# Optimization experiments

Measured on AMD Instinct MI355X. Metric: run time of the kernel, lower is better.

Reference implementation:

```python
import jax, jax.numpy as jnp
import numpy as np

# Constants from the torch module __init__
FACE_INDS = np.array([[0, 1, 2, 3], [0, 4, 2, 6], [0, 1, 4, 5],
                      [1, 3, 5, 7], [2, 3, 6, 7], [4, 5, 6, 7]])  # (6,4)
N_GRID = 11
N_POINTS = N_GRID * N_GRID        # 121
N_FACE = 6
N_KP_HAND = 21
N_CONTACTS = 10
ITA = 0.2
IND1 = np.array([0, 1, 2, 3])
IND2 = np.array([1, 2, 3, 0])


def _bilinear_grid():
    # grid[p, k] = bilinear weights for the 4 face corners, p over 11x11 (u,v)
    g = []
    for u in np.linspace(0.0, 1.0, N_GRID):
        for v in np.linspace(0.0, 1.0, N_GRID):
            g.append([v * (1 - u), v * u, (1 - v) * (1 - u), u * (1 - v)])
    return jnp.asarray(np.array(g, dtype=np.float32))  # (121, 4)


def setup_inputs() -> dict:
    key = jax.random.key(0)
    poses = jax.random.normal(key, (8192, N_KP_HAND + 8, 3), dtype=jnp.float32)
    return {"poses": poses}


def affinity_loss(poses):
    bs = poses.shape[0]
    hand = poses[:, :N_KP_HAND, :]          # (bs, 21, 3)
    obj = poses[:, N_KP_HAND:, :]           # (bs, 8, 3)

    # --- sample_face_points: bilinear sample 121 pts on each of the 6 faces ---
    grid = _bilinear_grid().astype(poses.dtype)        # (121, 4)
    faces = obj[:, FACE_INDS, :]                        # (bs, 6, 4, 3)
    face_points = jnp.einsum('bfkc,pk->bfpc', faces, grid)  # (bs, 6, 121, 3)
    obj_pts = face_points.reshape(bs, N_FACE * N_POINTS, 3)  # (bs, 726, 3)

    xx = jnp.sum(hand * hand, axis=-1)                  # (bs, 21)
    yy = jnp.sum(obj_pts * obj_pts, axis=-1)            # (bs, 726)
    zz = jnp.einsum('bic,bjc->bij', hand, obj_pts)      # (bs, 21, 726)
    pdist = jnp.sqrt(xx[:, :, None] + yy[:, None, :] - 2.0 * zz + 1e-6)
    pdist = pdist.reshape(bs, N_KP_HAND, N_FACE, N_POINTS)

    # --- per (hand kp, face) nearest face point, then global top-10 contacts ---
    dist_h2f = jnp.min(pdist, axis=3)                   # (bs, 21, 6)
    idxs_h2f = jnp.argmin(pdist, axis=3)                # (bs, 21, 6)
    flat = dist_h2f.reshape(bs, N_KP_HAND * N_FACE)     # (bs, 126)
    order = jnp.argsort(flat, axis=1)[:, :N_CONTACTS]   # (bs, 10)
    dist = jnp.take_along_axis(flat, order, axis=1)     # (bs, 10)
    inds_hand = order // N_FACE
    inds_face = order % N_FACE
    b = jnp.arange(bs)[:, None]
    ind_obj = idxs_h2f[b, inds_hand, inds_face]                     # (bs, 10)
    obj_contacts = obj_pts[b, inds_face * N_POINTS + ind_obj]       # (bs, 10, 3)

    # --- get_obj_info: axis endpoints and mean edge length of the bbox ---
    points1 = obj[:, :4, :].mean(axis=1)                # (bs, 3)
    points2 = obj[:, 4:, :].mean(axis=1)                # (bs, 3)
    l1 = jnp.linalg.norm(obj[:, IND1] - obj[:, IND2], axis=-1).mean(1, keepdims=True)
    l2 = jnp.linalg.norm(obj[:, IND1 + 4] - obj[:, IND2 + 4], axis=-1).mean(1, keepdims=True)
    length = (l1 + l2) * 0.5                            # (bs, 1)

    mask1 = (dist < length * ITA).astype(poses.dtype)   # (bs, 10)
    mask = mask1[:, :, None] * mask1[:, None, :]        # (bs, 10, 10)

    direct_vec = points2 - points1                      # (bs, 3)
    dv_norm = jnp.linalg.norm(direct_vec, axis=1, keepdims=True)  # (bs, 1)
    normed_dv = direct_vec / (dv_norm + 1e-5)
    vec_contacts = obj_contacts - points1[:, None, :]   # (bs, 10, 3)
    inner = jnp.sum(direct_vec[:, None, :] * vec_contacts, axis=-1)  # (bs, 10)
    t = inner / (dv_norm + 1e-5)                        # (bs, 10)
    r = points1[:, None, :] + normed_dv[:, None, :] * t[:, :, None]  # (bs, 10, 3)
    normal_vec = obj_contacts - r
    normal_vec = normal_vec / (jnp.linalg.norm(normal_vec, axis=2, keepdims=True) + 1e-5)
    cos_sim = jnp.einsum('bic,bjc->bij', normal_vec, normal_vec)  # (bs, 10, 10)

    return (cos_sim * mask).sum() / (mask.sum() + 1.0)


def reference(poses):
    return affinity_loss(poses)
```

## Files before the change

kernel.cpp:

```cpp
#include <hip/hip_runtime.h>
#include <math.h>

#define NGRID   11
#define NPAIR   126
#define NCONT   10

#define NSUB    64
#define NBUK    128
#define WS_SUB  16
#define WS_BUK  128
#define WS_WORDS (WS_BUK + 2 * NBUK)

#define NBUCKET 256

typedef float v2f __attribute__((ext_vector_type(2)));
#define FMA2(a,b,c) __builtin_elementwise_fma((a),(b),(c))
#define MAX2(a,b)   __builtin_elementwise_max((a),(b))
#define SP2(x)      ((v2f){(x),(x)})

__device__ __constant__ int4 c_face4[6] = {
    {0,1,2,3},{0,4,2,6},{0,1,4,5},{1,3,5,7},{2,3,6,7},{4,5,6,7}};
__device__ __constant__ float c_U[NGRID] = {
    0.0f,0.1f,0.2f,0.3f,0.4f,0.5f,0.6f,0.7f,0.8f,0.9f,1.0f};

__global__ void zero_ws_kernel(float* ws, int n) {
    int t = blockIdx.x * 256 + threadIdx.x;
    if (t < n) ws[t] = 0.0f;
}

__device__ __forceinline__ void coefs_from_face(
        const float4* __restrict__ Ff, float hx, float hy, float hz,
        float& C00, float& C10, float& C01, float& C11,
        float& C20, float& C02, float& C21, float& C12, float& C22) {
    const float4 F0 = Ff[0], F1 = Ff[1], F2 = Ff[2],
                 F3 = Ff[3], F4 = Ff[4], F5 = Ff[5];
    const float hx2 = 2.0f * hx, hy2 = 2.0f * hy, hz2 = 2.0f * hz;
    const float ha2 = fmaf(hx2, F0.x, fmaf(hy2, F0.y, hz2 * F0.z));
    const float hb2 = fmaf(hx2, F1.x, fmaf(hy2, F1.y, hz2 * F1.z));
    const float hc2 = fmaf(hx2, F2.x, fmaf(hy2, F2.y, hz2 * F2.z));
    const float hd2 = fmaf(hx2, F3.x, fmaf(hy2, F3.y, hz2 * F3.z));
    C00 = ha2 - F0.w;
    C10 = hb2 - F4.x;
    C01 = hc2 - F4.y;
    C11 = hd2 - F4.z;
    C20 = -F1.w;  C02 = -F2.w;  C21 = -F4.w;  C12 = -F5.x;  C22 = -F3.w;
}

__launch_bounds__(256)
__global__ void affinity_kernel(const float* __restrict__ poses,
                                float* __restrict__ ws,
                                float* __restrict__ out,
                                int bs, int mode) {
    const int t    = threadIdx.x;
    const int half = t >> 7;
    const int t0   = t & 127;
    const int batch = blockIdx.x * 2 + half;
    const bool valid = batch < bs;

    __shared__ float    sh_pose[2][88];
    __shared__ float4   sh_face[2][36];
    __shared__ float    sh_thr[2][2];
    __shared__ int      sh_ru[2][128];
    __shared__ int      sh_cpair[2][128];
    __shared__ unsigned sh_cnt[2], sh_cnt2[2];
    __shared__ unsigned sh_key[2][128];
    __shared__ float    sh_cont[2][128][3];
    __shared__ float    sh_win[2][NCONT][3];
    __shared__ float    sh_nd[2][2];
    __shared__ int      sh_last;
    __shared__ double   sh_rn[4], sh_rd[4];

    if (valid && t0 < 87) sh_pose[half][t0] = poses[(size_t)batch * 87 + t0];
    if (t0 == 127) { sh_cnt[half] = 0u; sh_cnt2[half] = 0u; }
    __syncthreads();

    const float* hand = sh_pose[half];
    const float* obj  = sh_pose[half] + 63;

    if (valid && t0 < 6) {
        const int4 F = c_face4[t0];
        float C0[3], C1[3], C2[3], C3[3];
        #pragma unroll
        for (int c = 0; c < 3; ++c) {
            C0[c] = obj[F.x * 3 + c];
            C1[c] = obj[F.y * 3 + c];
            C2[c] = obj[F.z * 3 + c];
            C3[c] = obj[F.w * 3 + c];
        }
        float av[3], bv[3], cv[3], dv[3];
        #pragma unroll
        for (int c = 0; c < 3; ++c) {
            av[c] = C2[c];
            bv[c] = C3[c] - C2[c];
            cv[c] = C0[c] - C2[c];
            dv[c] = C1[c] - C0[c] - C3[c] + C2[c];
        }
        float aa=0.f,bb=0.f,cc=0.f,dd=0.f,ab=0.f,ac=0.f,ad=0.f,bc=0.f,bd=0.f,cd=0.f;
        #pragma unroll
        for (int c = 0; c < 3; ++c) {
            aa += av[c]*av[c]; bb += bv[c]*bv[c];
            cc += cv[c]*cv[c]; dd += dv[c]*dv[c];
            ab += av[c]*bv[c]; ac += av[c]*cv[c];
            ad += av[c]*dv[c]; bc += bv[c]*cv[c];
            bd += bv[c]*dv[c]; cd += cv[c]*dv[c];
        }
        float4* Ff = &sh_face[half][t0 * 6];
        Ff[0] = make_float4(av[0], av[1], av[2], aa);
        Ff[1] = make_float4(bv[0], bv[1], bv[2], bb);
        Ff[2] = make_float4(cv[0], cv[1], cv[2], cc);
        Ff[3] = make_float4(dv[0], dv[1], dv[2], dd);
        Ff[4] = make_float4(2.f*ab, 2.f*ac, 2.f*(ad+bc), 2.f*bd);
        Ff[5] = make_float4(2.f*cd, 0.f, 0.f, 0.f);
    }
    if (valid && t0 == 6) {
        float l1 = 0.0f, l2 = 0.0f;
        #pragma unroll
        for (int e = 0; e < 4; ++e) {
            const int a = e, b2 = (e + 1) & 3;
            {
                const float dx = obj[a*3+0]-obj[b2*3+0];
                const float dy = obj[a*3+1]-obj[b2*3+1];
                const float dz = obj[a*3+2]-obj[b2*3+2];
                l1 += sqrtf(dx*dx + dy*dy + dz*dz);
            }
            {
                const float dx = obj[(a+4)*3+0]-obj[(b2+4)*3+0];
                const float dy = obj[(a+4)*3+1]-obj[(b2+4)*3+1];
                const float dz = obj[(a+4)*3+2]-obj[(b2+4)*3+2];
                l2 += sqrtf(dx*dx + dy*dy + dz*dz);
            }
        }
        l1 *= 0.25f; l2 *= 0.25f;
        const float L02 = (l1 + l2) * 0.5f * 0.2f;
        sh_thr[half][0] = L02 * L02 - 1e-6f + 1e-2f;
        sh_thr[half][1] = L02;
    }
    __syncthreads();

    if (valid && t0 < NPAIR) {
        const int i = t0 / 6;
        const int f = t0 - i * 6;
        const float hx = hand[i*3+0], hy = hand[i*3+1], hz = hand[i*3+2];
        const float xx = hx*hx + hy*hy + hz*hz;
        float C00,C10,C01,C11,C20,C02,C21,C12,C22;
        coefs_from_face(&sh_face[half][f*6], hx, hy, hz,
                        C00,C10,C01,C11,C20,C02,C21,C12,C22);

        const float U[NGRID] = {0.0f,0.1f,0.2f,0.3f,0.4f,0.5f,
                                0.6f,0.7f,0.8f,0.9f,1.0f};
        float qb = -3.0e38f;
        int   ru = 0;
        #pragma unroll
        for (int rp = 0; rp < 5; ++rp) {
            const v2f u2 = (v2f){U[2*rp], U[2*rp+1]};
            const v2f A2 = FMA2(FMA2(SP2(C22), u2, SP2(C12)), u2, SP2(C02));
            const v2f A1 = FMA2(FMA2(SP2(C21), u2, SP2(C11)), u2, SP2(C01));
            const v2f A0 = FMA2(FMA2(SP2(C20), u2, SP2(C10)), u2, SP2(C00));
            v2f m2 = A0;
            #pragma unroll
            for (int iv = 1; iv < NGRID; ++iv) {
                const v2f vv = SP2(U[iv]);
                m2 = MAX2(m2, FMA2(FMA2(A2, vv, A1), vv, A0));
            }
            if (m2.x > qb) { qb = m2.x; ru = 2*rp; }
            if (m2.y > qb) { qb = m2.y; ru = 2*rp + 1; }
        }
        {
            const float u = 1.0f;
            const float A2 = fmaf(fmaf(C22,u,C12),u,C02);
            const float A1 = fmaf(fmaf(C21,u,C11),u,C01);
            const float A0 = fmaf(fmaf(C20,u,C10),u,C00);
            float m1 = A0;
            #pragma unroll
            for (int iv = 1; iv < NGRID; ++iv)
                m1 = fmaxf(m1, fmaf(fmaf(A2,U[iv],A1),U[iv],A0));
            if (m1 > qb) { qb = m1; ru = 10; }
        }
        sh_ru[half][t0] = ru;
        const float d2s = xx - qb;
        if (d2s < sh_thr[half][0]) {
            const unsigned s = atomicAdd(&sh_cnt[half], 1u);
            sh_cpair[half][s] = t0;
        }
    }
    __syncthreads();

    {
        const int cnt = (int)sh_cnt[half];
        if (t0 < cnt) {
            const int pair = sh_cpair[half][t0];
            const int i  = pair / 6;
            const int f  = pair - 6 * i;
            const int ru = sh_ru[half][pair];
            const float hx = hand[i*3+0], hy = hand[i*3+1], hz = hand[i*3+2];
            float C00,C10,C01,C11,C20,C02,C21,C12,C22;
            coefs_from_face(&sh_face[half][f*6], hx, hy, hz,
                            C00,C10,C01,C11,C20,C02,C21,C12,C22);
            const float u  = c_U[ru];
            const float A2 = fmaf(fmaf(C22,u,C12),u,C02);
            const float A1 = fmaf(fmaf(C21,u,C11),u,C01);
            const float A0 = fmaf(fmaf(C20,u,C10),u,C00);
            const float U[NGRID] = {0.0f,0.1f,0.2f,0.3f,0.4f,0.5f,
                                    0.6f,0.7f,0.8f,0.9f,1.0f};
            float qr = A0; int vb = 0;
            #pragma unroll
            for (int iv = 1; iv < NGRID; ++iv) {
                const float q = fmaf(fmaf(A2,U[iv],A1),U[iv],A0);
                if (q > qr) { qr = q; vb = iv; }
            }
            const double du = ru * 0.1;
            const double dv = vb * 0.1;
            const float w0 = (float)(dv * (1.0 - du));
            const float w1 = (float)(dv * du);
            const float w2 = (float)((1.0 - dv) * (1.0 - du));
            const float w3 = (float)(du * (1.0 - dv));
            const int4 F = c_face4[f];
            const int i0 = F.x*3, i1 = F.y*3, i2 = F.z*3, i3 = F.w*3;
            const float cx = w0*obj[i0+0]+w1*obj[i1+0]+w2*obj[i2+0]+w3*obj[i3+0];
            const float cy = w0*obj[i0+1]+w1*obj[i1+1]+w2*obj[i2+1]+w3*obj[i3+1];
            const float cz = w0*obj[i0+2]+w1*obj[i1+2]+w2*obj[i2+2]+w3*obj[i3+2];
            const float xx = hx*hx + hy*hy + hz*hz;
            const float yy = cx*cx + cy*cy + cz*cz;
            const float zz = hx*cx + hy*cy + hz*cz;
            const float d2e = (xx + yy) - 2.0f * zz;
            const float dist = sqrtf(d2e + 1e-6f);
            if (dist < sh_thr[half][1]) {
                const unsigned s2 = atomicAdd(&sh_cnt2[half], 1u);
                const float d2k = fmaxf(d2e, 0.0f);
                sh_key[half][s2] = (__float_as_uint(d2k) & 0xFFFFFF80u)
                                 | (unsigned)pair;
                sh_cont[half][s2][0] = cx;
                sh_cont[half][s2][1] = cy;
                sh_cont[half][s2][2] = cz;
            }
        }
    }
    __syncthreads();

    const int n2 = (int)sh_cnt2[half];
    if (t0 < n2) {
        const unsigned ke = sh_key[half][t0];
        int rank = 0;
        for (int j = 0; j < n2; ++j) rank += (sh_key[half][j] < ke) ? 1 : 0;
        if (rank < NCONT) {
            sh_win[half][rank][0] = sh_cont[half][t0][0];
            sh_win[half][rank][1] = sh_cont[half][t0][1];
            sh_win[half][rank][2] = sh_cont[half][t0][2];
        }
    }
    __syncthreads();

    const int kwin = n2 < NCONT ? n2 : NCONT;
    float px = 0.f, py = 0.f, pz = 0.f;
    if (valid && t0 < kwin) {
        const float cx = sh_win[half][t0][0];
        const float cy = sh_win[half][t0][1];
        const float cz = sh_win[half][t0][2];
        const float p1x = (((obj[0] +obj[3]) +obj[6]) +obj[9]) *0.25f;
        const float p1y = (((obj[1] +obj[4]) +obj[7]) +obj[10])*0.25f;
        const float p1z = (((obj[2] +obj[5]) +obj[8]) +obj[11])*0.25f;
        const float p2x = (((obj[12]+obj[15])+obj[18])+obj[21])*0.25f;
        const float p2y = (((obj[13]+obj[16])+obj[19])+obj[22])*0.25f;
        const float p2z = (((obj[14]+obj[17])+obj[20])+obj[23])*0.25f;
        const float dvx = p2x-p1x, dvy = p2y-p1y, dvz = p2z-p1z;
        const float dvn = sqrtf(dvx*dvx + dvy*dvy + dvz*dvz);
        const float den = dvn + 1e-5f;
        const float ndx = dvx/den, ndy = dvy/den, ndz = dvz/den;
        const float vcx = cx-p1x, vcy = cy-p1y, vcz = cz-p1z;
        const float inner = dvx*vcx + dvy*vcy + dvz*vcz;
        const float tp = inner / den;
        const float rx = p1x + ndx*tp, ry = p1y + ndy*tp, rz = p1z + ndz*tp;
        float nvx = cx-rx, nvy = cy-ry, nvz = cz-rz;
        const float nvn = sqrtf(nvx*nvx + nvy*nvy + nvz*nvz) + 1e-5f;
        px = nvx / nvn; py = nvy / nvn; pz = nvz / nvn;
    }
    if (t0 < 64) {
        #pragma unroll
        for (int off = 32; off >= 1; off >>= 1) {
            px += __shfl_xor(px, off, 64);
            py += __shfl_xor(py, off, 64);
            pz += __shfl_xor(pz, off, 64);
        }
        if (t0 == 0) {
            sh_nd[half][0] = px*px + py*py + pz*pz;
            sh_nd[half][1] = (float)(kwin * kwin);
        }
    }
    __syncthreads();

    if (t == 0) {
        sh_last = 0;
        const float num = sh_nd[0][0] + sh_nd[1][0];
        const float dnm = sh_nd[0][1] + sh_nd[1][1];
        const int b = blockIdx.x;
        if (mode) {
            float* bkt = ws + WS_BUK + 2 * (b & (NBUK - 1));
            const float r0 = atomicAdd(bkt + 0, num);
            const float r1 = atomicAdd(bkt + 1, dnm);
            asm volatile("" :: "v"(r0), "v"(r1) : "memory");
            unsigned* subs = (unsigned*)ws + WS_SUB;
            const unsigned nb = gridDim.x;
            const unsigned g  = (unsigned)b & (NSUB - 1);
            const unsigned quota = (nb - 1u - g) / NSUB + 1u;
            const unsigned old = atomicAdd(subs + g, 1u);
            if (old + 1u == quota) {
                const unsigned ngroups = nb < NSUB ? nb : NSUB;
                const unsigned m2 = atomicAdd((unsigned*)ws, 1u);
                if (m2 + 1u == ngroups) sh_last = 1;
            }
        } else {
            float* bucket = ws + 2 * (b & (NBUCKET - 1));
            atomicAdd(bucket + 0, num);
            atomicAdd(bucket + 1, dnm);
        }
    }
    __syncthreads();

    if (sh_last) {
        double n = 0.0, d = 0.0;
        if (t < NBUK) {
            float* bkt = ws + WS_BUK + 2 * t;
            n = (double)atomicAdd(bkt + 0, 0.0f);
            d = (double)atomicAdd(bkt + 1, 0.0f);
        }
        #pragma unroll
        for (int off = 32; off >= 1; off >>= 1) {
            n += __shfl_xor(n, off, 64);
            d += __shfl_xor(d, off, 64);
        }
        const int w = t >> 6;
        if ((t & 63) == 0) { sh_rn[w] = n; sh_rd[w] = d; }
        __syncthreads();
        if (t == 0) {
            const double nn = sh_rn[0] + sh_rn[1] + sh_rn[2] + sh_rn[3];
            const double dd = sh_rd[0] + sh_rd[1] + sh_rd[2] + sh_rd[3];
            out[0] = (float)(nn / (dd + 1.0));
        }
    }
}

__launch_bounds__(1024)
__global__ void finalize_kernel(const float* __restrict__ ws,
                                float* __restrict__ out, int nslot) {
    const int t = threadIdx.x;
    __shared__ double sh_n[16], sh_d[16];
    double n = 0.0, d = 0.0;
    for (int k = t; k < nslot; k += 1024) {
        n += (double)ws[2 * k + 0];
        d += (double)ws[2 * k + 1];
    }
    #pragma unroll
    for (int off = 32; off >= 1; off >>= 1) {
        n += __shfl_xor(n, off, 64);
        d += __shfl_xor(d, off, 64);
    }
    const int w = t >> 6;
    if ((t & 63) == 0) { sh_n[w] = n; sh_d[w] = d; }
    __syncthreads();
    if (t == 0) {
        double nn = 0.0, dd = 0.0;
        #pragma unroll
        for (int i = 0; i < 16; ++i) { nn += sh_n[i]; dd += sh_d[i]; }
        out[0] = (float)(nn / (dd + 1.0));
    }
}

extern "C" void kernel_launch(void* const* d_in, const int* in_sizes, int n_in,
                              void* d_out, int out_size, void* d_ws, size_t ws_size,
                              hipStream_t stream) {
    const float* poses = (const float*)d_in[0];
    float* out = (float*)d_out;
    float* ws  = (float*)d_ws;
    const int bs = in_sizes[0] / 87;
    const int nblk = (bs + 1) / 2;

    if (ws_size >= (size_t)WS_WORDS * sizeof(float)) {
        hipMemsetAsync(ws, 0, WS_WORDS * sizeof(float), stream);
        hipLaunchKernelGGL(affinity_kernel, dim3(nblk), dim3(256), 0, stream,
                           poses, ws, out, bs, 1);
    } else {
        hipLaunchKernelGGL(zero_ws_kernel, dim3(1), dim3(256), 0, stream,
                           ws, NBUCKET * 2);
        hipLaunchKernelGGL(affinity_kernel, dim3(nblk), dim3(256), 0, stream,
                           poses, ws, out, bs, 0);
        hipLaunchKernelGGL(finalize_kernel, dim3(1), dim3(1024), 0, stream,
                           ws, out, NBUCKET);
    }
}
```

Baseline: 77.21 us.

## Map one batch element per wavefront, replacing block barriers with ballots

Each 64-lane wavefront now processes a whole batch element, with each lane scanning up to two (hand, face) pairs. All __syncthreads and shared atomics are replaced by wave ballots, popcount compaction and shuffles. Per-face coefficients are recomputed per pair in registers instead of staged in shared memory. This removes block barriers and shared-memory round trips, at the cost of redundant coefficient arithmetic and doubling the heavy scan per lane, with 4 elements per block instead of 2. The final global accumulation is done per wave.

After: 90.16 us. +16.8%, slower.

```diff
diff --git a/kernel.cpp b/kernel.cpp
--- a/kernel.cpp
+++ b/kernel.cpp
@@ -28,91 +28,116 @@
     if (t < n) ws[t] = 0.0f;
 }
 
-__device__ __forceinline__ void coefs_from_face(
-        const float4* __restrict__ Ff, float hx, float hy, float hz,
+__device__ __forceinline__ void pair_coefs(
+        const float* __restrict__ obj, float hx, float hy, float hz, int f,
         float& C00, float& C10, float& C01, float& C11,
         float& C20, float& C02, float& C21, float& C12, float& C22) {
-    const float4 F0 = Ff[0], F1 = Ff[1], F2 = Ff[2],
-                 F3 = Ff[3], F4 = Ff[4], F5 = Ff[5];
-    const float hx2 = 2.0f * hx, hy2 = 2.0f * hy, hz2 = 2.0f * hz;
-    const float ha2 = fmaf(hx2, F0.x, fmaf(hy2, F0.y, hz2 * F0.z));
-    const float hb2 = fmaf(hx2, F1.x, fmaf(hy2, F1.y, hz2 * F1.z));
-    const float hc2 = fmaf(hx2, F2.x, fmaf(hy2, F2.y, hz2 * F2.z));
-    const float hd2 = fmaf(hx2, F3.x, fmaf(hy2, F3.y, hz2 * F3.z));
-    C00 = ha2 - F0.w;
-    C10 = hb2 - F4.x;
-    C01 = hc2 - F4.y;
-    C11 = hd2 - F4.z;
-    C20 = -F1.w;  C02 = -F2.w;  C21 = -F4.w;  C12 = -F5.x;  C22 = -F3.w;
+    const int4 F = c_face4[f];
+    float av[3], bv[3], cv[3], dv[3];
+    #pragma unroll
+    for (int c = 0; c < 3; ++c) {
+        const float P0 = obj[F.x * 3 + c];
+        const float P1 = obj[F.y * 3 + c];
+        const float P2 = obj[F.z * 3 + c];
+        const float P3 = obj[F.w * 3 + c];
+        av[c] = P2;
+        bv[c] = P3 - P2;
+        cv[c] = P0 - P2;
+        dv[c] = P1 - P0 - P3 + P2;
+    }
+    float aa=0.f,bb=0.f,cc=0.f,dd=0.f,ab=0.f,ac=0.f,ad=0.f,bc=0.f,bd=0.f,cd=0.f;
+    #pragma unroll
+    for (int c = 0; c < 3; ++c) {
+        aa += av[c]*av[c]; bb += bv[c]*bv[c];
+        cc += cv[c]*cv[c]; dd += dv[c]*dv[c];
+        ab += av[c]*bv[c]; ac += av[c]*cv[c];
+        ad += av[c]*dv[c]; bc += bv[c]*cv[c];
+        bd += bv[c]*dv[c]; cd += cv[c]*dv[c];
+    }
+    const float hx2 = 2.0f*hx, hy2 = 2.0f*hy, hz2 = 2.0f*hz;
+    const float ha2 = fmaf(hx2, av[0], fmaf(hy2, av[1], hz2*av[2]));
+    const float hb2 = fmaf(hx2, bv[0], fmaf(hy2, bv[1], hz2*bv[2]));
+    const float hc2 = fmaf(hx2, cv[0], fmaf(hy2, cv[1], hz2*cv[2]));
+    const float hd2 = fmaf(hx2, dv[0], fmaf(hy2, dv[1], hz2*dv[2]));
+    C00 = ha2 - aa;
+    C10 = hb2 - 2.f*ab;
+    C01 = hc2 - 2.f*ac;
+    C11 = hd2 - 2.f*(ad + bc);
+    C20 = -bb;  C02 = -cc;  C21 = -2.f*bd;  C12 = -2.f*cd;  C22 = -dd;
+}
+
+__device__ __forceinline__ void scan_pair(
+        const float* __restrict__ obj, const float* __restrict__ hand,
+        int pair, float& d2s, int& ru_out) {
+    const int i = pair / 6;
+    const int f = pair - i * 6;
+    const float hx = hand[i*3+0], hy = hand[i*3+1], hz = hand[i*3+2];
+    const float xx = hx*hx + hy*hy + hz*hz;
+    float C00,C10,C01,C11,C20,C02,C21,C12,C22;
+    pair_coefs(obj, hx, hy, hz, f, C00,C10,C01,C11,C20,C02,C21,C12,C22);
+
+    const float U[NGRID] = {0.0f,0.1f,0.2f,0.3f,0.4f,0.5f,
+                            0.6f,0.7f,0.8f,0.9f,1.0f};
+    float qb = -3.0e38f;
+    int   ru = 0;
+    #pragma unroll
+    for (int rp = 0; rp < 5; ++rp) {
+        const v2f u2 = (v2f){U[2*rp], U[2*rp+1]};
+        const v2f A2 = FMA2(FMA2(SP2(C22), u2, SP2(C12)), u2, SP2(C02));
+        const v2f A1 = FMA2(FMA2(SP2(C21), u2, SP2(C11)), u2, SP2(C01));
+        const v2f A0 = FMA2(FMA2(SP2(C20), u2, SP2(C10)), u2, SP2(C00));
+        v2f m2 = A0;
+        #pragma unroll
+        for (int iv = 1; iv < NGRID; ++iv) {
+            const v2f vv = SP2(U[iv]);
+            m2 = MAX2(m2, FMA2(FMA2(A2, vv, A1), vv, A0));
+        }
+        if (m2.x > qb) { qb = m2.x; ru = 2*rp; }
+        if (m2.y > qb) { qb = m2.y; ru = 2*rp + 1; }
+    }
+    {
+        const float A2 = fmaf(fmaf(C22,1.f,C12),1.f,C02);
+        const float A1 = fmaf(fmaf(C21,1.f,C11),1.f,C01);
+        const float A0 = fmaf(fmaf(C20,1.f,C10),1.f,C00);
+        float m1 = A0;
+        #pragma unroll
+        for (int iv = 1; iv < NGRID; ++iv)
+            m1 = fmaxf(m1, fmaf(fmaf(A2,U[iv],A1),U[iv],A0));
+        if (m1 > qb) { qb = m1; ru = 10; }
+    }
+    d2s = xx - qb;
+    ru_out = ru;
 }
 
 __launch_bounds__(256)
 __global__ void affinity_kernel(const float* __restrict__ poses,
                                 float* __restrict__ ws,
                                 float* __restrict__ out,
-                                int bs, int mode) {
-    const int t    = threadIdx.x;
-    const int half = t >> 7;
-    const int t0   = t & 127;
-    const int batch = blockIdx.x * 2 + half;
-    const bool valid = batch < bs;
-
-    __shared__ float    sh_pose[2][88];
-    __shared__ float4   sh_face[2][36];
-    __shared__ float    sh_thr[2][2];
-    __shared__ int      sh_ru[2][128];
-    __shared__ int      sh_cpair[2][128];
-    __shared__ unsigned sh_cnt[2], sh_cnt2[2];
-    __shared__ unsigned sh_key[2][128];
-    __shared__ float    sh_cont[2][128][3];
-    __shared__ float    sh_win[2][NCONT][3];
-    __shared__ float    sh_nd[2][2];
-    __shared__ int      sh_last;
-    __shared__ double   sh_rn[4], sh_rd[4];
-
-    if (valid && t0 < 87) sh_pose[half][t0] = poses[(size_t)batch * 87 + t0];
-    if (t0 == 127) { sh_cnt[half] = 0u; sh_cnt2[half] = 0u; }
-    __syncthreads();
-
-    const float* hand = sh_pose[half];
-    const float* obj  = sh_pose[half] + 63;
-
-    if (valid && t0 < 6) {
-        const int4 F = c_face4[t0];
-        float C0[3], C1[3], C2[3], C3[3];
-        #pragma unroll
-        for (int c = 0; c < 3; ++c) {
-            C0[c] = obj[F.x * 3 + c];
-            C1[c] = obj[F.y * 3 + c];
-            C2[c] = obj[F.z * 3 + c];
-            C3[c] = obj[F.w * 3 + c];
-        }
-        float av[3], bv[3], cv[3], dv[3];
-        #pragma unroll
-        for (int c = 0; c < 3; ++c) {
-            av[c] = C2[c];
-            bv[c] = C3[c] - C2[c];
-            cv[c] = C0[c] - C2[c];
-            dv[c] = C1[c] - C0[c] - C3[c] + C2[c];
-        }
-        float aa=0.f,bb=0.f,cc=0.f,dd=0.f,ab=0.f,ac=0.f,ad=0.f,bc=0.f,bd=0.f,cd=0.f;
-        #pragma unroll
-        for (int c = 0; c < 3; ++c) {
-            aa += av[c]*av[c]; bb += bv[c]*bv[c];
-            cc += cv[c]*cv[c]; dd += dv[c]*dv[c];
-            ab += av[c]*bv[c]; ac += av[c]*cv[c];
-            ad += av[c]*dv[c]; bc += bv[c]*cv[c];
-            bd += bv[c]*dv[c]; cd += cv[c]*dv[c];
-        }
-        float4* Ff = &sh_face[half][t0 * 6];
-        Ff[0] = make_float4(av[0], av[1], av[2], aa);
-        Ff[1] = make_float4(bv[0], bv[1], bv[2], bb);
-        Ff[2] = make_float4(cv[0], cv[1], cv[2], cc);
-        Ff[3] = make_float4(dv[0], dv[1], dv[2], dd);
-        Ff[4] = make_float4(2.f*ab, 2.f*ac, 2.f*(ad+bc), 2.f*bd);
-        Ff[5] = make_float4(2.f*cd, 0.f, 0.f, 0.f);
-    }
-    if (valid && t0 == 6) {
+                                int bs, int nw, int mode) {
+    const int lane = threadIdx.x & 63;
+    const int wv   = threadIdx.x >> 6;
+    const int gw   = blockIdx.x * 4 + wv;
+    const bool valid = gw < bs;
+
+    __shared__ float    sh_pose[4][88];
+    __shared__ unsigned sh_cand[4][128];
+    __shared__ unsigned sh_keys[4][128];
+    float*    pose = sh_pose[wv];
+    unsigned* cand = sh_cand[wv];
+    unsigned* keys = sh_keys[wv];
+
+    if (valid) {
+        const float* src = poses + (size_t)gw * 87;
+        pose[lane] = src[lane];
+        if (lane < 23) pose[64 + lane] = src[64 + lane];
+    }
+    __threadfence_block();
+
+    float num = 0.f, dnm = 0.f;
+    if (valid) {
+        const float* hand = pose;
+        const float* obj  = pose + 63;
+
         float l1 = 0.0f, l2 = 0.0f;
         #pragma unroll
         for (int e = 0; e < 4; ++e) {
@@ -131,211 +156,173 @@
             }
         }
         l1 *= 0.25f; l2 *= 0.25f;
-        const float L02 = (l1 + l2) * 0.5f * 0.2f;
-        sh_thr[half][0] = L02 * L02 - 1e-6f + 1e-2f;
-        sh_thr[half][1] = L02;
-    }
-    __syncthreads();
-
-    if (valid && t0 < NPAIR) {
-        const int i = t0 / 6;
-        const int f = t0 - i * 6;
-        const float hx = hand[i*3+0], hy = hand[i*3+1], hz = hand[i*3+2];
-        const float xx = hx*hx + hy*hy + hz*hz;
-        float C00,C10,C01,C11,C20,C02,C21,C12,C22;
-        coefs_from_face(&sh_face[half][f*6], hx, hy, hz,
-                        C00,C10,C01,C11,C20,C02,C21,C12,C22);
-
-        const float U[NGRID] = {0.0f,0.1f,0.2f,0.3f,0.4f,0.5f,
-                                0.6f,0.7f,0.8f,0.9f,1.0f};
-        float qb = -3.0e38f;
-        int   ru = 0;
-        #pragma unroll
-        for (int rp = 0; rp < 5; ++rp) {
-            const v2f u2 = (v2f){U[2*rp], U[2*rp+1]};
-            const v2f A2 = FMA2(FMA2(SP2(C22), u2, SP2(C12)), u2, SP2(C02));
-            const v2f A1 = FMA2(FMA2(SP2(C21), u2, SP2(C11)), u2, SP2(C01));
-            const v2f A0 = FMA2(FMA2(SP2(C20), u2, SP2(C10)), u2, SP2(C00));
-            v2f m2 = A0;
+        const float L02  = (l1 + l2) * 0.5f * 0.2f;
+        const float thrF = L02 * L02 - 1e-6f + 1e-2f;
+
+        float d2A; int ruA;
+        scan_pair(obj, hand, lane, d2A, ruA);
+        const bool flagA = d2A < thrF;
+        const bool hasB  = (lane + 64) < NPAIR;
+        float d2B = 3.0e38f; int ruB = 0;
+        if (hasB) scan_pair(obj, hand, lane + 64, d2B, ruB);
+        const bool flagB = hasB && (d2B < thrF);
+
+        const unsigned long long lt = (1ull << lane) - 1ull;
+        const unsigned long long mA = __ballot(flagA);
+        const unsigned long long mB = __ballot(flagB);
+        const int cntA = __popcll(mA);
+        const int cnt  = cntA + __popcll(mB);
+        if (flagA) cand[__popcll(mA & lt)] =
+            (unsigned)lane | ((unsigned)ruA << 8);
+        if (flagB) cand[cntA + __popcll(mB & lt)] =
+            (unsigned)(lane + 64) | ((unsigned)ruB << 8);
+        __threadfence_block();
+
+        float rkey[2]; float rcx[2], rcy[2], rcz[2]; int rval[2] = {0, 0};
+        int n2 = 0;
+        #pragma unroll
+        for (int c = 0; c < 2; ++c) {
+            if (c == 1 && cnt <= 64) break;
+            const int idx = c * 64 + lane;
+            const bool act = idx < cnt;
+            bool pass = false; unsigned key = 0;
+            float cx = 0.f, cy = 0.f, cz = 0.f;
+            if (act) {
+                const unsigned rec = cand[idx];
+                const int pair = rec & 0xFF;
+                const int ru   = rec >> 8;
+                const int i = pair / 6;
+                const int f = pair - 6 * i;
+                const float hx = hand[i*3+0], hy = hand[i*3+1], hz = hand[i*3+2];
+                float C00,C10,C01,C11,C20,C02,C21,C12,C22;
+                pair_coefs(obj, hx, hy, hz, f,
+                           C00,C10,C01,C11,C20,C02,C21,C12,C22);
+                const float u  = c_U[ru];
+                const float A2 = fmaf(fmaf(C22,u,C12),u,C02);
+                const float A1 = fmaf(fmaf(C21,u,C11),u,C01);
+                const float A0 = fmaf(fmaf(C20,u,C10),u,C00);
+                const float U[NGRID] = {0.0f,0.1f,0.2f,0.3f,0.4f,0.5f,
+                                        0.6f,0.7f,0.8f,0.9f,1.0f};
+                float qr = A0; int vb = 0;
+                #pragma unroll
+                for (int iv = 1; iv < NGRID; ++iv) {
+                    const float q = fmaf(fmaf(A2,U[iv],A1),U[iv],A0);
+                    if (q > qr) { qr = q; vb = iv; }
+                }
+                const double du = ru * 0.1;
+                const double dv = vb * 0.1;
+                const float w0 = (float)(dv * (1.0 - du));
+                const float w1 = (float)(dv * du);
+                const float w2 = (float)((1.0 - dv) * (1.0 - du));
+                const float w3 = (float)(du * (1.0 - dv));
+                const int4 F = c_face4[f];
+                const int i0 = F.x*3, i1 = F.y*3, i2 = F.z*3, i3 = F.w*3;
+                cx = w0*obj[i0+0]+w1*obj[i1+0]+w2*obj[i2+0]+w3*obj[i3+0];
+                cy = w0*obj[i0+1]+w1*obj[i1+1]+w2*obj[i2+1]+w3*obj[i3+1];
+                cz = w0*obj[i0+2]+w1*obj[i1+2]+w2*obj[i2+2]+w3*obj[i3+2];
+                const float xx = hx*hx + hy*hy + hz*hz;
+                const float yy = cx*cx + cy*cy + cz*cz;
+                const float zz = hx*cx + hy*cy + hz*cz;
+                const float d2e = (xx + yy) - 2.0f * zz;
+                const float dist = sqrtf(d2e + 1e-6f);
+                pass = dist < L02;
+                key = (__float_as_uint(fmaxf(d2e, 0.0f)) & 0xFFFFFF80u)
+                    | (unsigned)pair;
+            }
+            const unsigned long long mp = __ballot(pass);
+            if (pass) {
+                keys[n2 + __popcll(mp & lt)] = key;
+                rkey[c] = __uint_as_float(key);
+                rcx[c] = cx; rcy[c] = cy; rcz[c] = cz;
+                rval[c] = 1;
+            }
+            n2 += __popcll(mp);
+        }
+        __threadfence_block();
+
+        const int kwin = n2 < NCONT ? n2 : NCONT;
+        float px = 0.f, py = 0.f, pz = 0.f;
+        if (rval[0] | rval[1]) {
+            const float p1x = (((obj[0] +obj[3]) +obj[6]) +obj[9]) *0.25f;
+            const float p1y = (((obj[1] +obj[4]) +obj[7]) +obj[10])*0.25f;
+            const float p1z = (((obj[2] +obj[5]) +obj[8]) +obj[11])*0.25f;
+            const float p2x = (((obj[12]+obj[15])+obj[18])+obj[21])*0.25f;
+            const float p2y = (((obj[13]+obj[16])+obj[19])+obj[22])*0.25f;
+            const float p2z = (((obj[14]+obj[17])+obj[20])+obj[23])*0.25f;
+            const float dvx = p2x-p1x, dvy = p2y-p1y, dvz = p2z-p1z;
+            const float dvn = sqrtf(dvx*dvx + dvy*dvy + dvz*dvz);
+            const float den = dvn + 1e-5f;
+            const float ndx = dvx/den, ndy = dvy/den, ndz = dvz/den;
             #pragma unroll
-            for (int iv = 1; iv < NGRID; ++iv) {
-                const v2f vv = SP2(U[iv]);
-                m2 = MAX2(m2, FMA2(FMA2(A2, vv, A1), vv, A0));
-            }
-            if (m2.x > qb) { qb = m2.x; ru = 2*rp; }
-            if (m2.y > qb) { qb = m2.y; ru = 2*rp + 1; }
-        }
-        {
-            const float u = 1.0f;
-            const float A2 = fmaf(fmaf(C22,u,C12),u,C02);
-            const float A1 = fmaf(fmaf(C21,u,C11),u,C01);
-            const float A0 = fmaf(fmaf(C20,u,C10),u,C00);
-            float m1 = A0;
-            #pragma unroll
-            for (int iv = 1; iv < NGRID; ++iv)
-                m1 = fmaxf(m1, fmaf(fmaf(A2,U[iv],A1),U[iv],A0));
-            if (m1 > qb) { qb = m1; ru = 10; }
-        }
-        sh_ru[half][t0] = ru;
-        const float d2s = xx - qb;
-        if (d2s < sh_thr[half][0]) {
-            const unsigned s = atomicAdd(&sh_cnt[half], 1u);
-            sh_cpair[half][s] = t0;
-        }
-    }
-    __syncthreads();
-
-    {
-        const int cnt = (int)sh_cnt[half];
-        if (t0 < cnt) {
-            const int pair = sh_cpair[half][t0];
-            const int i  = pair / 6;
-            const int f  = pair - 6 * i;
-            const int ru = sh_ru[half][pair];
-            const float hx = hand[i*3+0], hy = hand[i*3+1], hz = hand[i*3+2];
-            float C00,C10,C01,C11,C20,C02,C21,C12,C22;
-            coefs_from_face(&sh_face[half][f*6], hx, hy, hz,
-                            C00,C10,C01,C11,C20,C02,C21,C12,C22);
-            const float u  = c_U[ru];
-            const float A2 = fmaf(fmaf(C22,u,C12),u,C02);
-            const float A1 = fmaf(fmaf(C21,u,C11),u,C01);
-            const float A0 = fmaf(fmaf(C20,u,C10),u,C00);
-            const float U[NGRID] = {0.0f,0.1f,0.2f,0.3f,0.4f,0.5f,
-                                    0.6f,0.7f,0.8f,0.9f,1.0f};
-            float qr = A0; int vb = 0;
-            #pragma unroll
-            for (int iv = 1; iv < NGRID; ++iv) {
-                const float q = fmaf(fmaf(A2,U[iv],A1),U[iv],A0);
-                if (q > qr) { qr = q; vb = iv; }
-            }
-            const double du = ru * 0.1;
-            const double dv = vb * 0.1;
-            const float w0 = (float)(dv * (1.0 - du));
-            const float w1 = (float)(dv * du);
-            const float w2 = (float)((1.0 - dv) * (1.0 - du));
-            const float w3 = (float)(du * (1.0 - dv));
-            const int4 F = c_face4[f];
-            const int i0 = F.x*3, i1 = F.y*3, i2 = F.z*3, i3 = F.w*3;
-            const float cx = w0*obj[i0+0]+w1*obj[i1+0]+w2*obj[i2+0]+w3*obj[i3+0];
-            const float cy = w0*obj[i0+1]+w1*obj[i1+1]+w2*obj[i2+1]+w3*obj[i3+1];
-            const float cz = w0*obj[i0+2]+w1*obj[i1+2]+w2*obj[i2+2]+w3*obj[i3+2];
-            const float xx = hx*hx + hy*hy + hz*hz;
-            const float yy = cx*cx + cy*cy + cz*cz;
-            const float zz = hx*cx + hy*cy + hz*cz;
-            const float d2e = (xx + yy) - 2.0f * zz;
-            const float dist = sqrtf(d2e + 1e-6f);
-            if (dist < sh_thr[half][1]) {
-                const unsigned s2 = atomicAdd(&sh_cnt2[half], 1u);
-                const float d2k = fmaxf(d2e, 0.0f);
-                sh_key[half][s2] = (__float_as_uint(d2k) & 0xFFFFFF80u)
-                                 | (unsigned)pair;
-                sh_cont[half][s2][0] = cx;
-                sh_cont[half][s2][1] = cy;
-                sh_cont[half][s2][2] = cz;
-            }
-        }
-    }
-    __syncthreads();
-
-    const int n2 = (int)sh_cnt2[half];
-    if (t0 < n2) {
-        const unsigned ke = sh_key[half][t0];
-        int rank = 0;
-        for (int j = 0; j < n2; ++j) rank += (sh_key[half][j] < ke) ? 1 : 0;
-        if (rank < NCONT) {
-            sh_win[half][rank][0] = sh_cont[half][t0][0];
-            sh_win[half][rank][1] = sh_cont[half][t0][1];
-            sh_win[half][rank][2] = sh_cont[half][t0][2];
-        }
-    }
-    __syncthreads();
-
-    const int kwin = n2 < NCONT ? n2 : NCONT;
-    float px = 0.f, py = 0.f, pz = 0.f;
-    if (valid && t0 < kwin) {
-        const float cx = sh_win[half][t0][0];
-        const float cy = sh_win[half][t0][1];
-        const float cz = sh_win[half][t0][2];
-        const float p1x = (((obj[0] +obj[3]) +obj[6]) +obj[9]) *0.25f;
-        const float p1y = (((obj[1] +obj[4]) +obj[7]) +obj[10])*0.25f;
-        const float p1z = (((obj[2] +obj[5]) +obj[8]) +obj[11])*0.25f;
-        const float p2x = (((obj[12]+obj[15])+obj[18])+obj[21])*0.25f;
-        const float p2y = (((obj[13]+obj[16])+obj[19])+obj[22])*0.25f;
-        const float p2z = (((obj[14]+obj[17])+obj[20])+obj[23])*0.25f;
-        const float dvx = p2x-p1x, dvy = p2y-p1y, dvz = p2z-p1z;
-        const float dvn = sqrtf(dvx*dvx + dvy*dvy + dvz*dvz);
-        const float den = dvn + 1e-5f;
-        const float ndx = dvx/den, ndy = dvy/den, ndz = dvz/den;
-        const float vcx = cx-p1x, vcy = cy-p1y, vcz = cz-p1z;
-        const float inner = dvx*vcx + dvy*vcy + dvz*vcz;
-        const float tp = inner / den;
-        const float rx = p1x + ndx*tp, ry = p1y + ndy*tp, rz = p1z + ndz*tp;
-        float nvx = cx-rx, nvy = cy-ry, nvz = cz-rz;
-        const float nvn = sqrtf(nvx*nvx + nvy*nvy + nvz*nvz) + 1e-5f;
-        px = nvx / nvn; py = nvy / nvn; pz = nvz / nvn;
-    }
-    if (t0 < 64) {
+            for (int c = 0; c < 2; ++c) {
+                if (!rval[c]) continue;
+                const unsigned myk = __float_as_uint(rkey[c]);
+                int rank = 0;
+                for (int j = 0; j < n2; ++j) rank += (keys[j] < myk) ? 1 : 0;
+                if (rank < NCONT) {
+                    const float cx = rcx[c], cy = rcy[c], cz = rcz[c];
+                    const float vcx = cx-p1x, vcy = cy-p1y, vcz = cz-p1z;
+                    const float inner = dvx*vcx + dvy*vcy + dvz*vcz;
+                    const float tp = inner / den;
+                    const float rx = p1x + ndx*tp, ry = p1y + ndy*tp,
+                                rz = p1z + ndz*tp;
+                    const float nvx = cx-rx, nvy = cy-ry, nvz = cz-rz;
+                    const float nvn = sqrtf(nvx*nvx + nvy*nvy + nvz*nvz)
+                                    + 1e-5f;
+                    px += nvx / nvn; py += nvy / nvn; pz += nvz / nvn;
+                }
+            }
+        }
         #pragma unroll
         for (int off = 32; off >= 1; off >>= 1) {
             px += __shfl_xor(px, off, 64);
             py += __shfl_xor(py, off, 64);
             pz += __shfl_xor(pz, off, 64);
         }
-        if (t0 == 0) {
-            sh_nd[half][0] = px*px + py*py + pz*pz;
-            sh_nd[half][1] = (float)(kwin * kwin);
-        }
-    }
-    __syncthreads();
-
-    if (t == 0) {
-        sh_last = 0;
-        const float num = sh_nd[0][0] + sh_nd[1][0];
-        const float dnm = sh_nd[0][1] + sh_nd[1][1];
-        const int b = blockIdx.x;
+        if (lane == 0) {
+            num = px*px + py*py + pz*pz;
+            dnm = (float)(kwin * kwin);
+        }
+    }
+
+    int last = 0;
+    if (lane == 0) {
         if (mode) {
-            float* bkt = ws + WS_BUK + 2 * (b & (NBUK - 1));
+            float* bkt = ws + WS_BUK + 2 * (gw & (NBUK - 1));
             const float r0 = atomicAdd(bkt + 0, num);
             const float r1 = atomicAdd(bkt + 1, dnm);
             asm volatile("" :: "v"(r0), "v"(r1) : "memory");
             unsigned* subs = (unsigned*)ws + WS_SUB;
-            const unsigned nb = gridDim.x;
-            const unsigned g  = (unsigned)b & (NSUB - 1);
-            const unsigned quota = (nb - 1u - g) / NSUB + 1u;
+            const unsigned g = (unsigned)gw & (NSUB - 1);
+            const unsigned quota = ((unsigned)nw - 1u - g) / NSUB + 1u;
             const unsigned old = atomicAdd(subs + g, 1u);
             if (old + 1u == quota) {
-                const unsigned ngroups = nb < NSUB ? nb : NSUB;
+                const unsigned ngroups =
+                    (unsigned)nw < NSUB ? (unsigned)nw : NSUB;
                 const unsigned m2 = atomicAdd((unsigned*)ws, 1u);
-                if (m2 + 1u == ngroups) sh_last = 1;
+                if (m2 + 1u == ngroups) last = 1;
             }
         } else {
-            float* bucket = ws + 2 * (b & (NBUCKET - 1));
+            float* bucket = ws + 2 * (gw & (NBUCKET - 1));
             atomicAdd(bucket + 0, num);
             atomicAdd(bucket + 1, dnm);
         }
     }
-    __syncthreads();
-
-    if (sh_last) {
+    last = __shfl(last, 0, 64);
+
+    if (last) {
         double n = 0.0, d = 0.0;
-        if (t < NBUK) {
-            float* bkt = ws + WS_BUK + 2 * t;
-            n = (double)atomicAdd(bkt + 0, 0.0f);
-            d = (double)atomicAdd(bkt + 1, 0.0f);
+        for (int k = lane; k < NBUK; k += 64) {
+            float* bkt = ws + WS_BUK + 2 * k;
+            n += (double)atomicAdd(bkt + 0, 0.0f);
+            d += (double)atomicAdd(bkt + 1, 0.0f);
         }
         #pragma unroll
         for (int off = 32; off >= 1; off >>= 1) {
             n += __shfl_xor(n, off, 64);
             d += __shfl_xor(d, off, 64);
         }
-        const int w = t >> 6;
-        if ((t & 63) == 0) { sh_rn[w] = n; sh_rd[w] = d; }
-        __syncthreads();
-        if (t == 0) {
-            const double nn = sh_rn[0] + sh_rn[1] + sh_rn[2] + sh_rn[3];
-            const double dd = sh_rd[0] + sh_rd[1] + sh_rd[2] + sh_rd[3];
-            out[0] = (float)(nn / (dd + 1.0));
-        }
+        if (lane == 0) out[0] = (float)(n / (d + 1.0));
     }
 }
 
@@ -372,17 +359,18 @@
     float* out = (float*)d_out;
     float* ws  = (float*)d_ws;
     const int bs = in_sizes[0] / 87;
-    const int nblk = (bs + 1) / 2;
+    const int nblk = (bs + 3) / 4;
+    const int nw   = nblk * 4;
 
     if (ws_size >= (size_t)WS_WORDS * sizeof(float)) {
         hipMemsetAsync(ws, 0, WS_WORDS * sizeof(float), stream);
         hipLaunchKernelGGL(affinity_kernel, dim3(nblk), dim3(256), 0, stream,
-                           poses, ws, out, bs, 1);
+                           poses, ws, out, bs, nw, 1);
     } else {
         hipLaunchKernelGGL(zero_ws_kernel, dim3(1), dim3(256), 0, stream,
                            ws, NBUCKET * 2);
         hipLaunchKernelGGL(affinity_kernel, dim3(nblk), dim3(256), 0, stream,
-                           poses, ws, out, bs, 0);
+                           poses, ws, out, bs, nw, 0);
         hipLaunchKernelGGL(finalize_kernel, dim3(1), dim3(1024), 0, stream,
                            ws, out, NBUCKET);
     }
```
